# Performance work log

Hardware: AMD Instinct MI355X
Metric: run time of the kernel (lower is better)

Reference implementation:

```python
import jax, jax.numpy as jnp
import numpy as np

N = 100000      # num nodes
E = 3200000     # num edges (avg degree 32)
D = 64          # feature dim
K = 3           # propagation steps (self._k)
ALPHA = 0.1     # convex combine (self._alpha)
EPS = 1e-6      # PNY norm epsilon


def setup_inputs() -> dict:
    key = jax.random.key(0)
    k1, k2, k3 = jax.random.split(key, 3)
    feat = jax.random.normal(k1, (N, D), dtype=jnp.float32)
    src = jax.random.randint(k2, (E,), 0, N)
    dst = jax.random.randint(k3, (E,), 0, N)
    return {"feat": feat, "src": src, "dst": dst}


def reference(feat, src, dst):
    n = feat.shape[0]
    e = src.shape[0]
    ones = jnp.ones((e,), dtype=feat.dtype)
    out_deg = jax.ops.segment_sum(ones, src, num_segments=n)  # [N]
    in_deg = jax.ops.segment_sum(ones, dst, num_segments=n)   # [N]
    src_norm = jnp.power(jnp.clip(out_deg, 1.0, None), -0.5)[:, None]  # [N,1]
    dst_norm = jnp.power(jnp.clip(in_deg, 1.0, None), -0.5)[:, None]   # [N,1]

    feat_0 = feat
    for _ in range(K):
        feat = feat * src_norm                 # degree-norm scale on source side
        prev_x = feat                          # prev_x = clone(feat)
        # u_mul_e('h','w','m') with w==1 + fn.sum: edge-weighted sparse aggregation
        agg = jax.ops.segment_sum(feat[src], dst, num_segments=n)  # [N,D]
        # PNY_Norm(prev_x, agg): per-node L2-norm-preserving rescale of aggregate
        pn = jnp.linalg.norm(prev_x, axis=-1, keepdims=True)
        an = jnp.linalg.norm(agg, axis=-1, keepdims=True)
        feat = agg * (pn / (an + EPS))
        feat = feat * dst_norm                 # degree-norm scale on dest side
        feat = (1.0 - ALPHA) * feat + ALPHA * feat_0  # convex combine with feat_0
    return feat
```

## Files before the change

kernel.cpp:

```cpp
#include <hip/hip_runtime.h>
#include <hip/hip_fp16.h>
#include <math.h>

#define ALPHA 0.1f
#define EPS 1e-6f
#define D 64
#define CH 8192
#define BUCK_SH 8

__global__ void hist_kernel(const int* __restrict__ src, const int* __restrict__ dst,
                            int* __restrict__ hist_d, int* __restrict__ hist_s,
                            int nbuck, int nblk, int E) {
    __shared__ int hd[512], hs[512];
    int t = threadIdx.x, b = blockIdx.x;
    for (int u = t; u < 512; u += 256) { hd[u] = 0; hs[u] = 0; }
    __syncthreads();
    int beg = b * CH, end = min(beg + CH, E);
    for (int e = beg + t; e < end; e += 256) {
        atomicAdd(&hd[dst[e] >> BUCK_SH], 1);
        atomicAdd(&hs[src[e] >> BUCK_SH], 1);
    }
    __syncthreads();
    for (int u = t; u < nbuck; u += 256) {
        hist_d[u * nblk + b] = hd[u];
        hist_s[u * nblk + b] = hs[u];
    }
}

__global__ void bucket_total_kernel(const int* __restrict__ hist_d, const int* __restrict__ hist_s,
                                    int* __restrict__ tot_d, int* __restrict__ tot_s, int nblk) {
    __shared__ int rd[256], rs[256];
    int u = blockIdx.x, t = threadIdx.x;
    int sd = 0, ss = 0;
    for (int b = t; b < nblk; b += 256) {
        sd += hist_d[u * nblk + b];
        ss += hist_s[u * nblk + b];
    }
    rd[t] = sd; rs[t] = ss;
    __syncthreads();
    for (int off = 128; off; off >>= 1) {
        if (t < off) { rd[t] += rd[t + off]; rs[t] += rs[t + off]; }
        __syncthreads();
    }
    if (t == 0) { tot_d[u] = rd[0]; tot_s[u] = rs[0]; }
}

__global__ void base_scan_kernel(const int* __restrict__ tot_d, const int* __restrict__ tot_s,
                                 int* __restrict__ base_d, int* __restrict__ base_s, int nbuck) {
    __shared__ int a[512], b[512];
    int t = threadIdx.x;
    int vd = (t < nbuck) ? tot_d[t] : 0;
    int vs = (t < nbuck) ? tot_s[t] : 0;
    a[t] = vd; b[t] = vs;
    __syncthreads();
    for (int off = 1; off < 512; off <<= 1) {
        int av = (t >= off) ? a[t - off] : 0;
        int bv = (t >= off) ? b[t - off] : 0;
        __syncthreads();
        a[t] += av; b[t] += bv;
        __syncthreads();
    }
    if (t < nbuck) {
        base_d[t] = a[t] - vd;
        base_s[t] = b[t] - vs;
    }
}

__global__ void row_scan_kernel(const int* __restrict__ hist_d, const int* __restrict__ hist_s,
                                const int* __restrict__ base_d, const int* __restrict__ base_s,
                                int* __restrict__ sbase_d, int* __restrict__ sbase_s,
                                int nblk, int E, int m) {
    __shared__ int a[512], b[512];
    int u = blockIdx.x, t = threadIdx.x;
    int hd = (t < nblk) ? hist_d[u * nblk + t] : 0;
    int hs = (t < nblk) ? hist_s[u * nblk + t] : 0;
    a[t] = hd; b[t] = hs;
    __syncthreads();
    for (int off = 1; off < 512; off <<= 1) {
        int av = (t >= off) ? a[t - off] : 0;
        int bv = (t >= off) ? b[t - off] : 0;
        __syncthreads();
        a[t] += av; b[t] += bv;
        __syncthreads();
    }
    if (t < nblk) {
        sbase_d[u * nblk + t] = base_d[u] + a[t] - hd;
        sbase_s[u * nblk + t] = base_s[u] + b[t] - hs;
    }
    if (u == 0 && t == 0) { sbase_d[m] = E; sbase_s[m] = E; }
}

__global__ void scatter_kernel(const int* __restrict__ src, const int* __restrict__ dst,
                               const int* __restrict__ sbase_d, const int* __restrict__ sbase_s,
                               unsigned* __restrict__ pairs, unsigned char* __restrict__ skeys,
                               int nbuck, int nblk, int E) {
    __shared__ int cd[512], cs[512];
    int t = threadIdx.x, b = blockIdx.x;
    for (int u = t; u < nbuck; u += 256) {
        cd[u] = sbase_d[u * nblk + b];
        cs[u] = sbase_s[u * nblk + b];
    }
    __syncthreads();
    int beg = b * CH, end = min(beg + CH, E);
    for (int e = beg + t; e < end; e += 256) {
        int dv = dst[e], sv = src[e];
        int pu = atomicAdd(&cd[dv >> BUCK_SH], 1);
        pairs[pu] = ((unsigned)(dv & 255) << 24) | (unsigned)sv;
        int su = atomicAdd(&cs[sv >> BUCK_SH], 1);
        skeys[su] = (unsigned char)(sv & 255);
    }
}

__global__ void src_deg_kernel(const unsigned char* __restrict__ skeys,
                               const int* __restrict__ sbase_s,
                               float* __restrict__ sn, int nbuck, int nblk, int n) {
    __shared__ int lh[256];
    int t = threadIdx.x, u = blockIdx.x;
    lh[t] = 0;
    __syncthreads();
    int beg = sbase_s[u * nblk];
    int end = sbase_s[(u + 1) * nblk];
    for (int i = beg + t; i < end; i += 256) atomicAdd(&lh[skeys[i]], 1);
    __syncthreads();
    int node = (u << BUCK_SH) + t;
    if (node < n) sn[node] = rsqrtf(fmaxf((float)lh[t], 1.0f));
}

__global__ void build_kernel(const unsigned* __restrict__ pairs, const int* __restrict__ sbase_d,
                             int* __restrict__ rowptr, int* __restrict__ csr,
                             float* __restrict__ dn, int nbuck, int nblk, int n, int E) {
    __shared__ int lh[256], le[256], cnt[256];
    int t = threadIdx.x, u = blockIdx.x;
    lh[t] = 0; cnt[t] = 0;
    __syncthreads();
    int beg = sbase_d[u * nblk];
    int end = sbase_d[(u + 1) * nblk];
    for (int i = beg + t; i < end; i += 256) atomicAdd(&lh[pairs[i] >> 24], 1);
    __syncthreads();
    int c0 = lh[t];
    for (int off = 1; off < 256; off <<= 1) {
        int x = (t >= off) ? lh[t - off] : 0;
        __syncthreads();
        lh[t] += x;
        __syncthreads();
    }
    le[t] = lh[t] - c0;
    __syncthreads();
    int node = (u << BUCK_SH) + t;
    if (node < n) {
        rowptr[node] = beg + le[t];
        dn[node] = rsqrtf(fmaxf((float)c0, 1.0f));
    }
    if (u == nbuck - 1 && t == 0) rowptr[n] = E;
    for (int i = beg + t; i < end; i += 256) {
        unsigned pr = pairs[i];
        int bb = pr >> 24;
        int p = atomicAdd(&cnt[bb], 1);
        csr[beg + le[bb] + p] = (int)(pr & 0xFFFFFFu);
    }
}

__global__ void prescale_kernel(const float* __restrict__ feat, const float* __restrict__ sn,
                                __half* __restrict__ outh, float* __restrict__ pn, int n) {
    int row  = blockIdx.x * (blockDim.x >> 6) + (threadIdx.x >> 6);
    int lane = threadIdx.x & 63;
    if (row >= n) return;
    float x = feat[(long)row * D + lane];
    float ss = x * x;
    #pragma unroll
    for (int off = 32; off; off >>= 1) ss += __shfl_xor(ss, off, 64);
    float s = sn[row];
    float v = x * s;
    float vp = __shfl_xor(v, 1, 64);
    if (!(lane & 1)) {
        *(__half2*)(outh + (long)row * D + lane) = __floats2half2_rn(v, vp);
    }
    if (lane == 0) pn[row] = s * sqrtf(ss);
}

template <int LAST>
__global__ void iter_kernel(const __half* __restrict__ cur, const float* __restrict__ feat0,
                            const int* __restrict__ rowptr, const int* __restrict__ csr_src,
                            const float* __restrict__ pn, const float* __restrict__ dn,
                            const float* __restrict__ sn,
                            __half* __restrict__ nexth, float* __restrict__ npn,
                            float* __restrict__ out, int n) {
    int row  = blockIdx.x * (blockDim.x >> 6) + (threadIdx.x >> 6);
    int lane = threadIdx.x & 63;
    if (row >= n) return;
    int g = lane >> 3, sub = lane & 7;

    __half2 hz = __float2half2_rn(0.f);
    __half2 hacc0 = hz, hacc1 = hz, hacc2 = hz, hacc3 = hz;
    int beg = rowptr[row], end = rowptr[row + 1];
    for (int base = beg; base < end; base += 64) {
        int m = end - base; if (m > 64) m = 64;
        int s_l = (lane < m) ? csr_src[base + lane] : 0;
        int nfull = m >> 3;
        #pragma unroll 4
        for (int j = 0; j < nfull; ++j) {
            int s = __shfl(s_l, j * 8 + g, 64);
            int4 raw = *(const int4*)(cur + (long)s * D + sub * 8);
            hacc0 = __hadd2(hacc0, *(__half2*)&raw.x);
            hacc1 = __hadd2(hacc1, *(__half2*)&raw.y);
            hacc2 = __hadd2(hacc2, *(__half2*)&raw.z);
            hacc3 = __hadd2(hacc3, *(__half2*)&raw.w);
        }
        int e = nfull * 8 + g;
        int s = __shfl(s_l, e, 64);
        if (e < m) {
            int4 raw = *(const int4*)(cur + (long)s * D + sub * 8);
            hacc0 = __hadd2(hacc0, *(__half2*)&raw.x);
            hacc1 = __hadd2(hacc1, *(__half2*)&raw.y);
            hacc2 = __hadd2(hacc2, *(__half2*)&raw.z);
            hacc3 = __hadd2(hacc3, *(__half2*)&raw.w);
        }
    }
    float acc[8];
    { float2 f; f = __half22float2(hacc0); acc[0] = f.x; acc[1] = f.y;
      f = __half22float2(hacc1); acc[2] = f.x; acc[3] = f.y;
      f = __half22float2(hacc2); acc[4] = f.x; acc[5] = f.y;
      f = __half22float2(hacc3); acc[6] = f.x; acc[7] = f.y; }
    #pragma unroll
    for (int i = 0; i < 8; ++i) {
        float a = acc[i];
        a += __shfl_xor(a, 8, 64);
        a += __shfl_xor(a, 16, 64);
        a += __shfl_xor(a, 32, 64);
        acc[i] = a;
    }
    float dd = 0.f;
    #pragma unroll
    for (int i = 0; i < 8; ++i) dd += acc[i] * acc[i];
    dd += __shfl_xor(dd, 1, 64);
    dd += __shfl_xor(dd, 2, 64);
    dd += __shfl_xor(dd, 4, 64);
    float an = sqrtf(dd);
    float scale = pn[row] / (an + EPS) * dn[row] * (1.0f - ALPHA);

    if (g == 0) {
        long fb = (long)row * D + sub * 8;
        float4 f0a = *(const float4*)(feat0 + fb);
        float4 f0b = *(const float4*)(feat0 + fb + 4);
        float nx[8];
        nx[0] = acc[0] * scale + ALPHA * f0a.x;
        nx[1] = acc[1] * scale + ALPHA * f0a.y;
        nx[2] = acc[2] * scale + ALPHA * f0a.z;
        nx[3] = acc[3] * scale + ALPHA * f0a.w;
        nx[4] = acc[4] * scale + ALPHA * f0b.x;
        nx[5] = acc[5] * scale + ALPHA * f0b.y;
        nx[6] = acc[6] * scale + ALPHA * f0b.z;
        nx[7] = acc[7] * scale + ALPHA * f0b.w;
        if (LAST) {
            float4 o0 = {nx[0], nx[1], nx[2], nx[3]};
            float4 o1 = {nx[4], nx[5], nx[6], nx[7]};
            *(float4*)(out + fb) = o0;
            *(float4*)(out + fb + 4) = o1;
        } else {
            float s = sn[row];
            __half2 h0 = __floats2half2_rn(nx[0] * s, nx[1] * s);
            __half2 h1 = __floats2half2_rn(nx[2] * s, nx[3] * s);
            __half2 h2 = __floats2half2_rn(nx[4] * s, nx[5] * s);
            __half2 h3 = __floats2half2_rn(nx[6] * s, nx[7] * s);
            int4 packed;
            packed.x = *(int*)&h0; packed.y = *(int*)&h1;
            packed.z = *(int*)&h2; packed.w = *(int*)&h3;
            *(int4*)(nexth + fb) = packed;
            float nn = 0.f;
            #pragma unroll
            for (int i = 0; i < 8; ++i) nn += nx[i] * nx[i];
            nn += __shfl_xor(nn, 1, 64);
            nn += __shfl_xor(nn, 2, 64);
            nn += __shfl_xor(nn, 4, 64);
            if (sub == 0) npn[row] = s * sqrtf(nn);
        }
    }
}

extern "C" void kernel_launch(void* const* d_in, const int* in_sizes, int n_in,
                              void* d_out, int out_size, void* d_ws, size_t ws_size,
                              hipStream_t stream) {
    const float* feat = (const float*)d_in[0];
    const int*   src  = (const int*)d_in[1];
    const int*   dst  = (const int*)d_in[2];
    float* out = (float*)d_out;

    int n = in_sizes[0] / D;
    int E = in_sizes[1];

    int nbuck = (n + 255) >> BUCK_SH;
    int nblk  = (E + CH - 1) / CH;
    int m     = nbuck * nblk;

    int* hist_d  = (int*)d_ws;
    int* hist_s  = hist_d + m;
    int* sbase_d = hist_s + m;
    int* sbase_s = sbase_d + m + 1;
    int* tot_d   = sbase_s + m + 1;
    int* tot_s   = tot_d + 512;
    int* base_d  = tot_s + 512;
    int* base_s  = base_d + 512;
    int* rowptr  = base_s + 512;
    float* sn    = (float*)(rowptr + n + 1);
    float* dn    = sn + n;
    float* pn_a  = dn + n;
    float* pn_b  = pn_a + n;

    size_t used4 = (size_t)(4 * m + 2) + 2048 + 5 * (size_t)n + 1;
    size_t offP  = (used4 * 4 + 255) & ~(size_t)255;
    unsigned* pairs  = (unsigned*)((char*)d_ws + offP);
    __half* scaled_a = (__half*)((char*)d_ws + offP);
    __half* scaled_b = scaled_a + (size_t)n * D;
    size_t szP = 2 * (size_t)n * D * sizeof(__half);
    size_t offQ = (offP + szP + 255) & ~(size_t)255;
    unsigned char* skeys = (unsigned char*)d_ws + offQ;
    int* csr = (int*)((char*)d_ws + offQ);

    int eblocks = nblk;
    hist_kernel<<<eblocks, 256, 0, stream>>>(src, dst, hist_d, hist_s, nbuck, nblk, E);
    bucket_total_kernel<<<nbuck, 256, 0, stream>>>(hist_d, hist_s, tot_d, tot_s, nblk);
    base_scan_kernel<<<1, 512, 0, stream>>>(tot_d, tot_s, base_d, base_s, nbuck);
    row_scan_kernel<<<nbuck, 512, 0, stream>>>(hist_d, hist_s, base_d, base_s,
                                               sbase_d, sbase_s, nblk, E, m);
    scatter_kernel<<<eblocks, 256, 0, stream>>>(src, dst, sbase_d, sbase_s, pairs, skeys,
                                                nbuck, nblk, E);
    src_deg_kernel<<<nbuck, 256, 0, stream>>>(skeys, sbase_s, sn, nbuck, nblk, n);
    build_kernel<<<nbuck, 256, 0, stream>>>(pairs, sbase_d, rowptr, csr, dn, nbuck, nblk, n, E);

    int blocks = (n + 3) / 4;
    prescale_kernel<<<blocks, 256, 0, stream>>>(feat, sn, scaled_a, pn_a, n);
    iter_kernel<0><<<blocks, 256, 0, stream>>>(scaled_a, feat, rowptr, csr, pn_a, dn, sn,
                                               scaled_b, pn_b, nullptr, n);
    iter_kernel<0><<<blocks, 256, 0, stream>>>(scaled_b, feat, rowptr, csr, pn_b, dn, sn,
                                               scaled_a, pn_a, nullptr, n);
    iter_kernel<1><<<blocks, 256, 0, stream>>>(scaled_a, feat, rowptr, csr, pn_a, dn, sn,
                                               nullptr, nullptr, out, n);
}
```

Measured before the change: 326.4 us.

## Fuse source-degree count into CSR build and coarsely sort neighbors by source id

Merges the separate source-degree kernel into the CSR build kernel, removing one launch. The build kernel now keys each edge by destination node plus the top three bits of the source id, using 2048 shared counters and a two-level scan. Each row's neighbor list is therefore grouped into eight source ranges, which is meant to improve gather locality in the propagation iterations. The cost is more shared memory and scan work per block, which may lower occupancy in the build step.

```diff
diff --git a/kernel.cpp b/kernel.cpp
--- a/kernel.cpp
+++ b/kernel.cpp
@@ -111,52 +111,60 @@
     }
 }
 
-__global__ void src_deg_kernel(const unsigned char* __restrict__ skeys,
-                               const int* __restrict__ sbase_s,
-                               float* __restrict__ sn, int nbuck, int nblk, int n) {
-    __shared__ int lh[256];
+__global__ void build_kernel(const unsigned* __restrict__ pairs, const int* __restrict__ sbase_d,
+                             const unsigned char* __restrict__ skeys, const int* __restrict__ sbase_s,
+                             int* __restrict__ rowptr, int* __restrict__ csr,
+                             float* __restrict__ dn, float* __restrict__ sn,
+                             int nbuck, int nblk, int n, int E, int rsh) {
+    __shared__ int lh[2048];
+    __shared__ int cnt[2048];
+    __shared__ int lhs[256];
+    __shared__ int tsum[256];
     int t = threadIdx.x, u = blockIdx.x;
-    lh[t] = 0;
-    __syncthreads();
-    int beg = sbase_s[u * nblk];
-    int end = sbase_s[(u + 1) * nblk];
-    for (int i = beg + t; i < end; i += 256) atomicAdd(&lh[skeys[i]], 1);
-    __syncthreads();
-    int node = (u << BUCK_SH) + t;
-    if (node < n) sn[node] = rsqrtf(fmaxf((float)lh[t], 1.0f));
-}
-
-__global__ void build_kernel(const unsigned* __restrict__ pairs, const int* __restrict__ sbase_d,
-                             int* __restrict__ rowptr, int* __restrict__ csr,
-                             float* __restrict__ dn, int nbuck, int nblk, int n, int E) {
-    __shared__ int lh[256], le[256], cnt[256];
-    int t = threadIdx.x, u = blockIdx.x;
-    lh[t] = 0; cnt[t] = 0;
-    __syncthreads();
+    for (int i = t; i < 2048; i += 256) { lh[i] = 0; cnt[i] = 0; }
+    lhs[t] = 0;
+    __syncthreads();
+    int sb = sbase_s[u * nblk];
+    int se = sbase_s[(u + 1) * nblk];
+    for (int i = sb + t; i < se; i += 256) atomicAdd(&lhs[skeys[i]], 1);
     int beg = sbase_d[u * nblk];
     int end = sbase_d[(u + 1) * nblk];
-    for (int i = beg + t; i < end; i += 256) atomicAdd(&lh[pairs[i] >> 24], 1);
-    __syncthreads();
-    int c0 = lh[t];
+    for (int i = beg + t; i < end; i += 256) {
+        unsigned pr = pairs[i];
+        int key = (int)((pr >> 24) << 3) | (int)((pr & 0xFFFFFFu) >> rsh);
+        atomicAdd(&lh[key], 1);
+    }
+    __syncthreads();
+    int base = t * 8, run = 0;
+    #pragma unroll
+    for (int k = 0; k < 8; ++k) { int v = lh[base + k]; lh[base + k] = run; run += v; }
+    tsum[t] = run;
+    __syncthreads();
     for (int off = 1; off < 256; off <<= 1) {
-        int x = (t >= off) ? lh[t - off] : 0;
-        __syncthreads();
-        lh[t] += x;
-        __syncthreads();
-    }
-    le[t] = lh[t] - c0;
+        int v = (t >= off) ? tsum[t - off] : 0;
+        __syncthreads();
+        tsum[t] += v;
+        __syncthreads();
+    }
+    int add = (t == 0) ? 0 : tsum[t - 1];
+    #pragma unroll
+    for (int k = 0; k < 8; ++k) lh[base + k] += add;
     __syncthreads();
     int node = (u << BUCK_SH) + t;
     if (node < n) {
-        rowptr[node] = beg + le[t];
-        dn[node] = rsqrtf(fmaxf((float)c0, 1.0f));
+        int r0 = lh[t * 8];
+        int r1 = (t == 255) ? (end - beg) : lh[(t + 1) * 8];
+        rowptr[node] = beg + r0;
+        dn[node] = rsqrtf(fmaxf((float)(r1 - r0), 1.0f));
+        sn[node] = rsqrtf(fmaxf((float)lhs[t], 1.0f));
     }
     if (u == nbuck - 1 && t == 0) rowptr[n] = E;
     for (int i = beg + t; i < end; i += 256) {
         unsigned pr = pairs[i];
-        int bb = pr >> 24;
-        int p = atomicAdd(&cnt[bb], 1);
-        csr[beg + le[bb] + p] = (int)(pr & 0xFFFFFFu);
+        unsigned sv = pr & 0xFFFFFFu;
+        int key = (int)((pr >> 24) << 3) | (int)(sv >> rsh);
+        int p = atomicAdd(&cnt[key], 1);
+        csr[beg + lh[key] + p] = (int)sv;
     }
 }
 
@@ -291,6 +299,8 @@
     int nbuck = (n + 255) >> BUCK_SH;
     int nblk  = (E + CH - 1) / CH;
     int m     = nbuck * nblk;
+    int rsh = 0;
+    while (((n - 1) >> rsh) >= 8) ++rsh;
 
     int* hist_d  = (int*)d_ws;
     int* hist_s  = hist_d + m;
@@ -324,8 +334,8 @@
                                                sbase_d, sbase_s, nblk, E, m);
     scatter_kernel<<<eblocks, 256, 0, stream>>>(src, dst, sbase_d, sbase_s, pairs, skeys,
                                                 nbuck, nblk, E);
-    src_deg_kernel<<<nbuck, 256, 0, stream>>>(skeys, sbase_s, sn, nbuck, nblk, n);
-    build_kernel<<<nbuck, 256, 0, stream>>>(pairs, sbase_d, rowptr, csr, dn, nbuck, nblk, n, E);
+    build_kernel<<<nbuck, 256, 0, stream>>>(pairs, sbase_d, skeys, sbase_s,
+                                            rowptr, csr, dn, sn, nbuck, nblk, n, E, rsh);
 
     int blocks = (n + 3) / 4;
     prescale_kernel<<<blocks, 256, 0, stream>>>(feat, sn, scaled_a, pn_a, n);
```

Measured after the change: 325.6 us. No clear change (-0.2%).

## Stage scatter in shared memory and fuse source-degree pass into build

Applied to the files above, without the earlier changes.

The scatter kernel now sorts each chunk by bucket in LDS (a local histogram and scan, then local placement) and writes pairs and source keys back to global memory in contiguous runs, found by binary search over the local offsets. The goal is to replace scattered per-edge global writes with more coalesced ones. The histogram kernel uses per-wave private LDS histograms to reduce atomic contention. The separate source-degree kernel is folded into the build kernel, saving one launch and one pass. In exchange the scatter kernel recomputes the histogram, uses about 45KB of LDS (lower occupancy), and adds scan and search overhead.

```diff
diff --git a/kernel.cpp b/kernel.cpp
--- a/kernel.cpp
+++ b/kernel.cpp
@@ -11,19 +11,22 @@
 __global__ void hist_kernel(const int* __restrict__ src, const int* __restrict__ dst,
                             int* __restrict__ hist_d, int* __restrict__ hist_s,
                             int nbuck, int nblk, int E) {
-    __shared__ int hd[512], hs[512];
-    int t = threadIdx.x, b = blockIdx.x;
-    for (int u = t; u < 512; u += 256) { hd[u] = 0; hs[u] = 0; }
+    __shared__ int hd[4][512], hs[4][512];
+    int t = threadIdx.x, b = blockIdx.x, w = t >> 6;
+    for (int u = t; u < 512; u += 256) {
+        hd[0][u] = 0; hd[1][u] = 0; hd[2][u] = 0; hd[3][u] = 0;
+        hs[0][u] = 0; hs[1][u] = 0; hs[2][u] = 0; hs[3][u] = 0;
+    }
     __syncthreads();
     int beg = b * CH, end = min(beg + CH, E);
     for (int e = beg + t; e < end; e += 256) {
-        atomicAdd(&hd[dst[e] >> BUCK_SH], 1);
-        atomicAdd(&hs[src[e] >> BUCK_SH], 1);
+        atomicAdd(&hd[w][dst[e] >> BUCK_SH], 1);
+        atomicAdd(&hs[w][src[e] >> BUCK_SH], 1);
     }
     __syncthreads();
     for (int u = t; u < nbuck; u += 256) {
-        hist_d[u * nblk + b] = hd[u];
-        hist_s[u * nblk + b] = hs[u];
+        hist_d[u * nblk + b] = hd[0][u] + hd[1][u] + hd[2][u] + hd[3][u];
+        hist_s[u * nblk + b] = hs[0][u] + hs[1][u] + hs[2][u] + hs[3][u];
     }
 }
 
@@ -94,45 +97,81 @@
                                const int* __restrict__ sbase_d, const int* __restrict__ sbase_s,
                                unsigned* __restrict__ pairs, unsigned char* __restrict__ skeys,
                                int nbuck, int nblk, int E) {
-    __shared__ int cd[512], cs[512];
+    __shared__ unsigned sp[CH];
+    __shared__ unsigned char sk[CH];
+    __shared__ int hd[512], hs[512];
+    __shared__ int ld[512], ls[512];
+    __shared__ int ts[256];
     int t = threadIdx.x, b = blockIdx.x;
-    for (int u = t; u < nbuck; u += 256) {
-        cd[u] = sbase_d[u * nblk + b];
-        cs[u] = sbase_s[u * nblk + b];
-    }
-    __syncthreads();
-    int beg = b * CH, end = min(beg + CH, E);
+    for (int u = t; u < 512; u += 256) { hd[u] = 0; hs[u] = 0; }
+    __syncthreads();
+    int beg = b * CH, end = min(beg + CH, E), cnt = end - beg;
+    for (int e = beg + t; e < end; e += 256) {
+        atomicAdd(&hd[dst[e] >> BUCK_SH], 1);
+        atomicAdd(&hs[src[e] >> BUCK_SH], 1);
+    }
+    __syncthreads();
+    int v0 = hd[2 * t], v1 = hd[2 * t + 1];
+    int w0 = hs[2 * t], w1 = hs[2 * t + 1];
+    ts[t] = v0 + v1;
+    __syncthreads();
+    for (int off = 1; off < 256; off <<= 1) {
+        int v = (t >= off) ? ts[t - off] : 0;
+        __syncthreads();
+        ts[t] += v;
+        __syncthreads();
+    }
+    int based = (t == 0) ? 0 : ts[t - 1];
+    ld[2 * t] = based; ld[2 * t + 1] = based + v0;
+    __syncthreads();
+    ts[t] = w0 + w1;
+    __syncthreads();
+    for (int off = 1; off < 256; off <<= 1) {
+        int v = (t >= off) ? ts[t - off] : 0;
+        __syncthreads();
+        ts[t] += v;
+        __syncthreads();
+    }
+    int bases = (t == 0) ? 0 : ts[t - 1];
+    ls[2 * t] = bases; ls[2 * t + 1] = bases + w0;
+    __syncthreads();
+    hd[2 * t] = ld[2 * t]; hd[2 * t + 1] = ld[2 * t + 1];
+    hs[2 * t] = ls[2 * t]; hs[2 * t + 1] = ls[2 * t + 1];
+    __syncthreads();
     for (int e = beg + t; e < end; e += 256) {
         int dv = dst[e], sv = src[e];
-        int pu = atomicAdd(&cd[dv >> BUCK_SH], 1);
-        pairs[pu] = ((unsigned)(dv & 255) << 24) | (unsigned)sv;
-        int su = atomicAdd(&cs[sv >> BUCK_SH], 1);
-        skeys[su] = (unsigned char)(sv & 255);
-    }
-}
-
-__global__ void src_deg_kernel(const unsigned char* __restrict__ skeys,
-                               const int* __restrict__ sbase_s,
-                               float* __restrict__ sn, int nbuck, int nblk, int n) {
-    __shared__ int lh[256];
+        int p = atomicAdd(&hd[dv >> BUCK_SH], 1);
+        sp[p] = ((unsigned)(dv & 255) << 24) | (unsigned)sv;
+        int q = atomicAdd(&hs[sv >> BUCK_SH], 1);
+        sk[q] = (unsigned char)(sv & 255);
+    }
+    __syncthreads();
+    for (int i = t; i < cnt; i += 256) {
+        unsigned pv = sp[i];
+        int lo = 0;
+        #pragma unroll
+        for (int s = 256; s; s >>= 1) { int mid = lo + s; if (mid < 512 && ld[mid] <= i) lo = mid; }
+        pairs[sbase_d[lo * nblk + b] + (i - ld[lo])] = pv;
+        unsigned char kv = sk[i];
+        int lo2 = 0;
+        #pragma unroll
+        for (int s = 256; s; s >>= 1) { int mid = lo2 + s; if (mid < 512 && ls[mid] <= i) lo2 = mid; }
+        skeys[sbase_s[lo2 * nblk + b] + (i - ls[lo2])] = kv;
+    }
+}
+
+__global__ void build_kernel(const unsigned* __restrict__ pairs, const int* __restrict__ sbase_d,
+                             const unsigned char* __restrict__ skeys, const int* __restrict__ sbase_s,
+                             int* __restrict__ rowptr, int* __restrict__ csr,
+                             float* __restrict__ dn, float* __restrict__ sn,
+                             int nbuck, int nblk, int n, int E) {
+    __shared__ int lh[256], le[256], cnt[256], lhs[256];
     int t = threadIdx.x, u = blockIdx.x;
-    lh[t] = 0;
-    __syncthreads();
-    int beg = sbase_s[u * nblk];
-    int end = sbase_s[(u + 1) * nblk];
-    for (int i = beg + t; i < end; i += 256) atomicAdd(&lh[skeys[i]], 1);
-    __syncthreads();
-    int node = (u << BUCK_SH) + t;
-    if (node < n) sn[node] = rsqrtf(fmaxf((float)lh[t], 1.0f));
-}
-
-__global__ void build_kernel(const unsigned* __restrict__ pairs, const int* __restrict__ sbase_d,
-                             int* __restrict__ rowptr, int* __restrict__ csr,
-                             float* __restrict__ dn, int nbuck, int nblk, int n, int E) {
-    __shared__ int lh[256], le[256], cnt[256];
-    int t = threadIdx.x, u = blockIdx.x;
-    lh[t] = 0; cnt[t] = 0;
-    __syncthreads();
+    lh[t] = 0; cnt[t] = 0; lhs[t] = 0;
+    __syncthreads();
+    int sb = sbase_s[u * nblk];
+    int se = sbase_s[(u + 1) * nblk];
+    for (int i = sb + t; i < se; i += 256) atomicAdd(&lhs[skeys[i]], 1);
     int beg = sbase_d[u * nblk];
     int end = sbase_d[(u + 1) * nblk];
     for (int i = beg + t; i < end; i += 256) atomicAdd(&lh[pairs[i] >> 24], 1);
@@ -150,6 +189,7 @@
     if (node < n) {
         rowptr[node] = beg + le[t];
         dn[node] = rsqrtf(fmaxf((float)c0, 1.0f));
+        sn[node] = rsqrtf(fmaxf((float)lhs[t], 1.0f));
     }
     if (u == nbuck - 1 && t == 0) rowptr[n] = E;
     for (int i = beg + t; i < end; i += 256) {
@@ -324,8 +364,8 @@
                                                sbase_d, sbase_s, nblk, E, m);
     scatter_kernel<<<eblocks, 256, 0, stream>>>(src, dst, sbase_d, sbase_s, pairs, skeys,
                                                 nbuck, nblk, E);
-    src_deg_kernel<<<nbuck, 256, 0, stream>>>(skeys, sbase_s, sn, nbuck, nblk, n);
-    build_kernel<<<nbuck, 256, 0, stream>>>(pairs, sbase_d, rowptr, csr, dn, nbuck, nblk, n, E);
+    build_kernel<<<nbuck, 256, 0, stream>>>(pairs, sbase_d, skeys, sbase_s,
+                                            rowptr, csr, dn, sn, nbuck, nblk, n, E);
 
     int blocks = (n + 3) / 4;
     prescale_kernel<<<blocks, 256, 0, stream>>>(feat, sn, scaled_a, pn_a, n);
```

New measurement: 301.6 us. 7.6% less time.
